# Kernel tuning notes

Hardware: AMD Instinct MI355X
Metric: run time of the kernel (lower is better)

Reference implementation:

```python
import jax, jax.numpy as jnp
import numpy as np

NUM_HEADS = 32
HEAD_DIM = 64
ROPE_THETA = 10000.0


def _rope_cos_sin(position_ids, head_dim, theta):
    # inv_freq: [head_dim/2]
    half = head_dim // 2
    inv_freq = 1.0 / (theta ** (jnp.arange(0, half, dtype=jnp.float32) * 2.0 / head_dim))
    angles = position_ids.astype(jnp.float32)[..., None] * inv_freq  # [B,S,half]
    return jnp.cos(angles), jnp.sin(angles)


def _apply_rope(x, cos, sin):
    # x: [B,S,H,hd]; cos/sin: [B,S,half] -> broadcast over heads (rotate-half, Llama style)
    half = x.shape[-1] // 2
    x1, x2 = x[..., :half], x[..., half:]
    c = cos[:, :, None, :]
    s = sin[:, :, None, :]
    return jnp.concatenate([x1 * c - x2 * s, x2 * c + x1 * s], axis=-1)


def setup_inputs() -> dict:
    key = jax.random.key(0)
    ks = jax.random.split(key, 8)
    B, S, D = 2, 2048, 2048
    hidden_states = jax.random.normal(ks[0], (B, S, D), dtype=jnp.float32)
    # causal additive mask (is_causal=False in IpexSDP; mask carries causality)
    causal = jnp.tril(jnp.ones((S, S), dtype=jnp.bool_))
    attention_mask = jnp.where(causal, 0.0, -1e9).astype(jnp.float32)[None, None, :, :]
    attention_mask = jnp.broadcast_to(attention_mask, (B, 1, S, S))
    position_ids = jnp.broadcast_to(jnp.arange(S, dtype=jnp.int64)[None, :], (B, S))
    scale = 0.02
    qkv_w = jax.random.normal(ks[1], (3, D, D), dtype=jnp.float32) * scale
    qkv_b = jax.random.normal(ks[2], (3, D), dtype=jnp.float32) * scale
    o_w = jax.random.normal(ks[3], (D, D), dtype=jnp.float32) * scale
    o_b = jax.random.normal(ks[4], (D,), dtype=jnp.float32) * scale
    residual = jax.random.normal(ks[5], (B, S, D), dtype=jnp.float32)
    return {
        'hidden_states': hidden_states,
        'attention_mask': attention_mask,
        'position_ids': position_ids,
        'qkv_w': qkv_w,
        'qkv_b': qkv_b,
        'o_w': o_w,
        'o_b': o_b,
        'residual': residual,
    }


def reference(hidden_states, attention_mask, position_ids, qkv_w, qkv_b, o_w, o_b, residual):
    B, S, D = hidden_states.shape
    H, hd = NUM_HEADS, HEAD_DIM
    # fused QKV projection (weights stored transposed: x @ W), matching mm_qkv_out
    qkv = jnp.einsum('bsd,tde->tbse', hidden_states, qkv_w) + qkv_b[:, None, None, :]
    q = qkv[0].reshape(B, S, H, hd)
    k = qkv[1].reshape(B, S, H, hd)
    v = qkv[2].reshape(B, S, H, hd)
    cos, sin = _rope_cos_sin(position_ids, hd, ROPE_THETA)
    q = _apply_rope(q, cos, sin)
    k = _apply_rope(k, cos, sin)
    scale = 1.0 / jnp.sqrt(jnp.asarray(hd, dtype=hidden_states.dtype))
    # [B,H,S,S]
    scores = jnp.einsum('bqhd,bkhd->bhqk', q, k) * scale + attention_mask
    probs = jax.nn.softmax(scores, axis=-1)
    attn = jnp.einsum('bhqk,bkhd->bqhd', probs, v).reshape(B, S, D)
    # o-proj fused with bias + residual add (matmul_add_add)
    out = attn @ o_w + o_b + residual
    return out
```

## Files before the change

### kernel.cpp

```cpp
#include <hip/hip_runtime.h>
#include <stdint.h>
#include <stdio.h>

#define D_MODEL 2048
#define SEQ     2048
#define NHEADS  32
#define HDIM    64
#define BATCH   2
#define BH      (BATCH * NHEADS)
#define GK      2048
#define NT      (GK / 64)

typedef unsigned short u16;
typedef unsigned int   u32;
typedef __attribute__((ext_vector_type(8))) short short8;
typedef __attribute__((ext_vector_type(4))) short s16x4;
typedef __attribute__((ext_vector_type(4))) float f32x4;
typedef __attribute__((ext_vector_type(4))) u32   u32x4;
typedef __attribute__((ext_vector_type(2))) u32   u32x2;

__device__ __forceinline__ float bf2f(u16 x) {
  union { u32 u; float f; } c; c.u = ((u32)x) << 16; return c.f;
}
__device__ __forceinline__ u16 f2bf(float f) {
  union { float f; u32 u; } c; c.f = f;
  u32 u = c.u;
  return (u16)((u + 0x7FFFu + ((u >> 16) & 1u)) >> 16);
}
__device__ __forceinline__ u32 fbits(float f) {
  union { float f; u32 u; } c; c.f = f; return c.u;
}

typedef const __attribute__((address_space(1))) u32* gas_t;
typedef __attribute__((address_space(3))) u32* las_t;
__device__ __forceinline__ void gll16(const void* g, void* l) {
  __builtin_amdgcn_global_load_lds((gas_t)g, (las_t)l, 16, 0, 0);
}
__device__ __forceinline__ u32 lds_addr(const void* p) {
  return (u32)(size_t)(const __attribute__((address_space(3))) void*)p;
}
template <int OFF>
__device__ __forceinline__ short8 ds_read128o(u32 addr) {
  short8 r;
  asm volatile("ds_read_b128 %0, %1 offset:%2" : "=v"(r) : "v"(addr), "i"(OFF));
  return r;
}

#define SBAR0 __builtin_amdgcn_sched_barrier(0)

__device__ __forceinline__ void swiz_mn(int pid, int nx, int& mtile, int& ntile) {
  int chunk = 8 * nx;
  int grp = pid / chunk, loc = pid - grp * chunk;
  mtile = grp * 8 + (loc & 7);
  ntile = loc >> 3;
}

__global__ __launch_bounds__(256) void cvt_k(const float* __restrict__ in,
                                             u16* __restrict__ out) {
  int id = blockIdx.x * 256 + threadIdx.x;
  f32x4 v = *(const f32x4*)&in[(size_t)id * 4];
  alignas(8) u16 o[4];
#pragma unroll
  for (int j = 0; j < 4; j++) o[j] = f2bf(v[j]);
  *(u32x2*)&out[(size_t)id * 4] = *(const u32x2*)o;
}

__global__ __launch_bounds__(256) void transpose_cvt_k(const float* __restrict__ qkv_w,
                                                       const float* __restrict__ o_w,
                                                       u16* __restrict__ outT) {
  __shared__ u16 tile[64][72];
  const int z = blockIdx.z;
  const float* inz = (z < 3) ? qkv_w + (size_t)z * D_MODEL * D_MODEL : o_w;
  u16* outz = outT + (size_t)z * D_MODEL * D_MODEL;
  const int r0 = blockIdx.y * 64, c0 = blockIdx.x * 64;
  const int t = threadIdx.x;
  const int lrow = t >> 4, lcol4 = (t & 15) * 4;
#pragma unroll
  for (int i = 0; i < 4; i++) {
    int r = lrow + i * 16;
    f32x4 v = *(const f32x4*)&inz[(size_t)(r0 + r) * D_MODEL + (c0 + lcol4)];
#pragma unroll
    for (int j = 0; j < 4; j++) tile[r][lcol4 + j] = f2bf(v[j]);
  }
  __syncthreads();
  const int row = t >> 3, col8 = (t & 7) * 8;
#pragma unroll
  for (int i = 0; i < 2; i++) {
    int r = row + i * 32;
    alignas(16) u16 vals[8];
#pragma unroll
    for (int j = 0; j < 8; j++) vals[j] = tile[col8 + j][r];
    *(u32x4*)&outz[(size_t)(c0 + r) * D_MODEL + (r0 + col8)] = *(const u32x4*)vals;
  }
}

__device__ __forceinline__ void stage_half(const u16* __restrict__ src, int rowbase, int k0,
                                           u16* tile, int h, int w, int srl, int scol) {
  u16* ldsb = tile + h * (128 * 64);
  const u16* g0 = &src[(size_t)(rowbase + h * 128 + srl) * GK + k0 + scol];
  const u16* g1 = &src[(size_t)(rowbase + h * 128 + srl + 8) * GK + k0 + scol];
  gll16(g0, (char*)ldsb + w * 2048);
  gll16(g1, (char*)ldsb + w * 2048 + 1024);
}

__device__ __forceinline__ void rd8(short8 dst[4][2], u32 base, u32 cq0, u32 cq1) {
  u32 b0 = base + cq0, b1 = base + cq1;
  dst[0][0] = ds_read128o<0>(b0);    dst[0][1] = ds_read128o<0>(b1);
  dst[1][0] = ds_read128o<2048>(b0); dst[1][1] = ds_read128o<2048>(b1);
  dst[2][0] = ds_read128o<4096>(b0); dst[2][1] = ds_read128o<4096>(b1);
  dst[3][0] = ds_read128o<6144>(b0); dst[3][1] = ds_read128o<6144>(b1);
}

template <int NFLO>
__device__ __forceinline__ void mfma_half(const short8 afc[4][2], const short8 bfc[4][2],
                                          f32x4 acc[4][4]) {
  __builtin_amdgcn_s_setprio(1);
#pragma unroll
  for (int mf = 0; mf < 4; mf++)
#pragma unroll
    for (int nf = NFLO; nf < NFLO + 2; nf++) {
      acc[mf][nf] = __builtin_amdgcn_mfma_f32_16x16x32_bf16(afc[mf][0], bfc[nf][0], acc[mf][nf], 0, 0, 0);
      acc[mf][nf] = __builtin_amdgcn_mfma_f32_16x16x32_bf16(afc[mf][1], bfc[nf][1], acc[mf][nf], 0, 0, 0);
    }
  __builtin_amdgcn_s_setprio(0);
}

#define KT_BODY(KT_, AFC, BFC, AFN, BFN)                                        \
  do {                                                                           \
    if ((KT_) + 1 < NT) rd8(AFN, asb + (u32)ri * (u32)(128 * 64 * 2) + rowA, cq0, cq1); \
    if ((KT_) + 1 < NT) { asm volatile("s_waitcnt lgkmcnt(8)"); }                \
    else                { asm volatile("s_waitcnt lgkmcnt(0)"); }                \
    SBAR0;                                                                       \
    mfma_half<0>(AFC, BFC, acc);                                                 \
    if ((KT_) + 1 < NT) rd8(BFN, bsb + (u32)ri * (u32)(256 * 64 * 2) + rowB, cq0, cq1); \
    SBAR0;                                                                       \
    mfma_half<2>(AFC, BFC, acc);                                                 \
    __builtin_amdgcn_s_barrier();                                                \
    SBAR0;                                                                       \
    if ((KT_) + 3 < NT) {                                                        \
      const int k3_ = ((KT_) + 3) * 64;                                          \
      stage_half(Ag, m0, k3_, AsB + si * (128 * 64), 0, w, srl, scol);           \
      stage_half(Bg, n0, k3_, BsB + si * (256 * 64), 0, w, srl, scol);           \
      stage_half(Bg, n0, k3_, BsB + si * (256 * 64), 1, w, srl, scol);           \
      asm volatile("s_waitcnt vmcnt(6)");                                        \
    } else {                                                                     \
      asm volatile("s_waitcnt vmcnt(0)");                                        \
    }                                                                            \
    SBAR0;                                                                       \
    __builtin_amdgcn_s_barrier();                                                \
    SBAR0;                                                                       \
    { int th_ = 3 - si - ri; si = ri; ri = th_; }                                \
  } while (0)

__device__ __forceinline__ void gemm_128x256(const u16* __restrict__ Ag,
                                             const u16* __restrict__ Bg,
                                             int m0, int n0,
                                             u16* AsB, u16* BsB,
                                             f32x4 acc[4][4]) {
  const int t = threadIdx.x, w = t >> 6, lane = t & 63;
  const int quad = lane >> 4, l16 = lane & 15;
  const int wr = w >> 2, wc = w & 3;
  const int srl = w * 16 + (lane >> 3);
  const int scol = (((lane & 7) ^ (lane >> 3)) << 3);
  const u32 asb = lds_addr(AsB), bsb = lds_addr(BsB);
  const u32 xorc = (u32)((l16 & 7) << 4);
  const u32 cq0 = (u32)(quad * 16) ^ xorc;
  const u32 cq1 = (u32)(64 + quad * 16) ^ xorc;
  const u32 rowA = (u32)((wr * 64 + l16) * 128);
  const u32 rowB = (u32)((wc * 64 + l16) * 128);

#pragma unroll
  for (int mf = 0; mf < 4; mf++)
#pragma unroll
    for (int nf = 0; nf < 4; nf++)
#pragma unroll
      for (int i = 0; i < 4; i++) acc[mf][nf][i] = 0.0f;

#pragma unroll
  for (int tt = 0; tt < 3; tt++) {
    stage_half(Ag, m0, tt * 64, AsB + tt * (128 * 64), 0, w, srl, scol);
    stage_half(Bg, n0, tt * 64, BsB + tt * (256 * 64), 0, w, srl, scol);
    stage_half(Bg, n0, tt * 64, BsB + tt * (256 * 64), 1, w, srl, scol);
  }
  asm volatile("s_waitcnt vmcnt(6)");
  SBAR0;
  __builtin_amdgcn_s_barrier();
  SBAR0;

  short8 af0[4][2], bf0[4][2], af1[4][2], bf1[4][2];
  rd8(af0, asb + rowA, cq0, cq1);
  rd8(bf0, bsb + rowB, cq0, cq1);
  int si = 0, ri = 1;

  for (int kt = 0; kt < NT; kt += 2) {
    KT_BODY(kt,     af0, bf0, af1, bf1);
    KT_BODY(kt + 1, af1, bf1, af0, bf0);
  }
}

__global__ __launch_bounds__(512, 1) void qkv_gemm_k(const u16* __restrict__ A,
                                                     const u16* __restrict__ BT,
                                                     const float* __restrict__ bias,
                                                     u16* __restrict__ Qb, u16* __restrict__ Kb,
                                                     u16* __restrict__ Vbt) {
  __shared__ u16 As[3][128 * 64];
  __shared__ u16 Bs[3][256 * 64];
  f32x4 acc[4][4];
  int mtile, ntile;
  swiz_mn(blockIdx.x, 24, mtile, ntile);
  const int m0 = mtile * 128, n0 = ntile * 256;
  gemm_128x256(A, BT, m0, n0, &As[0][0], &Bs[0][0], acc);

  const int t = threadIdx.x, lane = t & 63, quad = lane >> 4, l16 = lane & 15;
  const int w = t >> 6, wr = w >> 2, wc = w & 3;
  const int tsel = n0 >> 11;
  if (tsel < 2) {
    u16* dst = tsel ? Kb : Qb;
#pragma unroll
    for (int p = 0; p < 2; p++) {
      int nlo = n0 + wc * 64 + p * 16 + l16;
      float blo = bias[nlo], bhi = bias[nlo + 32];
      int j = p * 16 + l16;
      float inv = __expf((float)j * -0.28782313662425572f);
      int h = (nlo & 2047) >> 6;
#pragma unroll
      for (int mf = 0; mf < 4; mf++) {
#pragma unroll
        for (int r = 0; r < 4; r++) {
          int m = m0 + wr * 64 + mf * 16 + quad * 4 + r;
          int b = m >> 11, s = m & (SEQ - 1);
          float sn, cs;
          __sincosf((float)s * inv, &sn, &cs);
          float x1 = acc[mf][p][r] + blo;
          float x2 = acc[mf][p + 2][r] + bhi;
          size_t base = ((size_t)((b * NHEADS + h) * SEQ + s)) * HDIM;
          dst[base + j]      = f2bf(x1 * cs - x2 * sn);
          dst[base + j + 32] = f2bf(x2 * cs + x1 * sn);
        }
      }
    }
  } else {
#pragma unroll
    for (int nf = 0; nf < 4; nf++) {
      int n = n0 + wc * 64 + nf * 16 + l16;
      float bv = bias[n];
      int e = n & 2047, h = e >> 6, d = e & 63;
#pragma unroll
      for (int mf = 0; mf < 4; mf++) {
        int m0r = m0 + wr * 64 + mf * 16 + quad * 4;
        int b = m0r >> 11, s0 = m0r & (SEQ - 1);
        alignas(8) u16 o4[4];
#pragma unroll
        for (int r = 0; r < 4; r++) o4[r] = f2bf(acc[mf][nf][r] + bv);
        *(u32x2*)&Vbt[((size_t)((b * NHEADS + h) * HDIM + d)) * SEQ + s0] = *(const u32x2*)o4;
      }
    }
  }
}

__global__ __launch_bounds__(512, 1) void oproj_gemm_k(const u16* __restrict__ A,
                                                       const u16* __restrict__ BT,
                                                       const float* __restrict__ bias,
                                                       const float* __restrict__ resid,
                                                       float* __restrict__ out) {
  __shared__ u16 As[3][128 * 64];
  __shared__ u16 Bs[3][256 * 64];
  f32x4 acc[4][4];
  int mtile, ntile;
  swiz_mn(blockIdx.x, 8, mtile, ntile);
  const int m0 = mtile * 128, n0 = ntile * 256;
  gemm_128x256(A, BT, m0, n0, &As[0][0], &Bs[0][0], acc);

  const int t = threadIdx.x, lane = t & 63, quad = lane >> 4, l16 = lane & 15;
  const int w = t >> 6, wr = w >> 2, wc = w & 3;
#pragma unroll
  for (int nf = 0; nf < 4; nf++) {
    int n = n0 + wc * 64 + nf * 16 + l16;
    float bv = bias[n];
#pragma unroll
    for (int mf = 0; mf < 4; mf++) {
#pragma unroll
      for (int r = 0; r < 4; r++) {
        int m = m0 + wr * 64 + mf * 16 + quad * 4 + r;
        size_t oi = (size_t)m * D_MODEL + n;
        out[oi] = acc[mf][nf][r] + bv + resid[oi];
      }
    }
  }
}

#define ATT_BUF (128 * 72 + 64 * 136)

__global__ __launch_bounds__(256, 2) void attn_k(const u16* __restrict__ Qb,
                                                 const u16* __restrict__ Kb,
                                                 const u16* __restrict__ Vbt,
                                                 u16* __restrict__ attn) {
  __shared__ u16 smem[2 * ATT_BUF];
  const int blk = blockIdx.x;
  const int bh = blk & 63, pi = blk >> 6;
  const int b = bh >> 5, h = bh & 31;
  const int t = threadIdx.x, w = t >> 6, lane = t & 63, quad = lane >> 4, l16 = lane & 15;
  const int qbT[2] = { pi * 128, (15 - pi) * 128 };
  const int qwT[2] = { qbT[0] + w * 32, qbT[1] + w * 32 };
  const size_t bho = (size_t)bh * SEQ * HDIM;
  const size_t vbo = (size_t)bh * HDIM * SEQ;
  const int kend = qbT[1] + 128;
  const int nr = kend >> 7;

  short8 qf[2][2][2];
#pragma unroll
  for (int Ti = 0; Ti < 2; Ti++)
#pragma unroll
    for (int qt = 0; qt < 2; qt++)
#pragma unroll
      for (int kd = 0; kd < 2; kd++) {
        short8 v = *(const short8*)&Qb[bho + (size_t)(qwT[Ti] + qt * 16 + l16) * HDIM + kd * 32 + quad * 8];
#pragma unroll
        for (int i = 0; i < 8; i++) {
          float f = bf2f((u16)v[i]) * 0.125f;
          v[i] = (short)f2bf(f);
        }
        qf[Ti][qt][kd] = v;
      }

  f32x4 Oacc[2][4][2];
  float mrow[2][2] = {{-1e30f, -1e30f}, {-1e30f, -1e30f}};
  float lrow[2][2] = {{0.0f, 0.0f}, {0.0f, 0.0f}};
#pragma unroll
  for (int Ti = 0; Ti < 2; Ti++)
#pragma unroll
    for (int dt = 0; dt < 4; dt++)
#pragma unroll
      for (int qt = 0; qt < 2; qt++)
#pragma unroll
        for (int i = 0; i < 4; i++) Oacc[Ti][dt][qt][i] = 0.0f;

  const int krow = t >> 3, kcol = (t & 7) * 8;
  u32x4 kreg[4], vreg[4];

#pragma unroll
  for (int c = 0; c < 4; c++) {
    kreg[c] = *(const u32x4*)&Kb[bho + (size_t)(krow + c * 32) * HDIM + kcol];
    int id = t + c * 256, vrow = id >> 4, vcol = (id & 15) * 8;
    vreg[c] = *(const u32x4*)&Vbt[vbo + (size_t)vrow * SEQ + vcol];
  }
  {
    u16* Ks = smem;
    u16* Vt = smem + 128 * 72;
#pragma unroll
    for (int c = 0; c < 4; c++) {
      *(u32x4*)&Ks[(krow + c * 32) * 72 + kcol] = kreg[c];
      int id = t + c * 256, vrow = id >> 4, vcol = (id & 15) * 8;
      *(u32x4*)&Vt[vrow * 136 + vcol] = vreg[c];
    }
  }
  __syncthreads();

  for (int r = 0; r < nr; r++) {
    const int key0 = r << 7;
    const int cur = r & 1;
    u16* Ks = smem + cur * ATT_BUF;
    u16* Vt = Ks + 128 * 72;
    if (r + 1 < nr) {
      const int nk0 = key0 + 128;
#pragma unroll
      for (int c = 0; c < 4; c++) {
        kreg[c] = *(const u32x4*)&Kb[bho + (size_t)(nk0 + krow + c * 32) * HDIM + kcol];
        int id = t + c * 256, vrow = id >> 4, vcol = (id & 15) * 8;
        vreg[c] = *(const u32x4*)&Vbt[vbo + (size_t)vrow * SEQ + nk0 + vcol];
      }
    }
#pragma unroll
    for (int s = 0; s < 2; s++) {
      const int k0s = key0 + s * 64;
      const int so = s * 64;
#pragma unroll
      for (int Ti = 0; Ti < 2; Ti++) {
        const int qw = qwT[Ti];
        if (k0s <= qw + 31) {
          const int lim = qw + 31 - k0s;
          int nkt = (lim >> 4) + 1; if (nkt > 4) nkt = 4;
          f32x4 sacc[4][2];
#pragma unroll
          for (int kt = 0; kt < 4; kt++) {
            if (kt < nkt) {
              short8 kf0 = *(const short8*)&Ks[(so + kt * 16 + l16) * 72 + quad * 8];
              short8 kf1 = *(const short8*)&Ks[(so + kt * 16 + l16) * 72 + 32 + quad * 8];
#pragma unroll
              for (int qt = 0; qt < 2; qt++) {
                f32x4 z = {0.0f, 0.0f, 0.0f, 0.0f};
                z = __builtin_amdgcn_mfma_f32_16x16x32_bf16(kf0, qf[Ti][qt][0], z, 0, 0, 0);
                z = __builtin_amdgcn_mfma_f32_16x16x32_bf16(kf1, qf[Ti][qt][1], z, 0, 0, 0);
                sacc[kt][qt] = z;
              }
            }
          }
          if (k0s + 63 > qw) {
#pragma unroll
            for (int qt = 0; qt < 2; qt++) {
              int qrow = qw + qt * 16 + l16;
#pragma unroll
              for (int kt = 0; kt < 4; kt++)
                if (kt < nkt)
#pragma unroll
                  for (int rr = 0; rr < 4; rr++)
                    if (k0s + kt * 16 + quad * 4 + rr > qrow) sacc[kt][qt][rr] = -1e30f;
            }
          }
          float alpha[2];
#pragma unroll
          for (int qt = 0; qt < 2; qt++) {
            float mx = -1e30f;
#pragma unroll
            for (int kt = 0; kt < 4; kt++)
              if (kt < nkt)
#pragma unroll
                for (int rr = 0; rr < 4; rr++) mx = fmaxf(mx, sacc[kt][qt][rr]);
            mx = fmaxf(mx, __shfl_xor(mx, 16));
            mx = fmaxf(mx, __shfl_xor(mx, 32));
            float mnew = fmaxf(mrow[Ti][qt], mx);
            alpha[qt] = __expf(mrow[Ti][qt] - mnew);
            mrow[Ti][qt] = mnew;
            float rsum = 0.0f;
#pragma unroll
            for (int kt = 0; kt < 4; kt++)
              if (kt < nkt)
#pragma unroll
                for (int rr = 0; rr < 4; rr++) {
                  float pv = __expf(sacc[kt][qt][rr] - mnew);
                  sacc[kt][qt][rr] = pv;
                  rsum += pv;
                }
            rsum += __shfl_xor(rsum, 16);
            rsum += __shfl_xor(rsum, 32);
            lrow[Ti][qt] = lrow[Ti][qt] * alpha[qt] + rsum;
          }
#pragma unroll
          for (int dt = 0; dt < 4; dt++)
#pragma unroll
            for (int qt = 0; qt < 2; qt++)
#pragma unroll
              for (int rr = 0; rr < 4; rr++) Oacc[Ti][dt][qt][rr] *= alpha[qt];
#pragma unroll
          for (int kt = 0; kt < 4; kt++) {
            if (kt < nkt) {
              s16x4 pk[2];
#pragma unroll
              for (int qt = 0; qt < 2; qt++) {
                u32 a0 = fbits(sacc[kt][qt][0]) + 0x8000u;
                u32 a1 = fbits(sacc[kt][qt][1]) + 0x8000u;
                u32 a2 = fbits(sacc[kt][qt][2]) + 0x8000u;
                u32 a3 = fbits(sacc[kt][qt][3]) + 0x8000u;
                union { u32 u[2]; s16x4 s; } pc;
                pc.u[0] = __builtin_amdgcn_perm(a1, a0, 0x07060302u);
                pc.u[1] = __builtin_amdgcn_perm(a3, a2, 0x07060302u);
                pk[qt] = pc.s;
              }
              s16x4 vf[4];
#pragma unroll
              for (int dt = 0; dt < 4; dt++)
                vf[dt] = *(const s16x4*)&Vt[(dt * 16 + l16) * 136 + so + kt * 16 + quad * 4];
#pragma unroll
              for (int dt = 0; dt < 4; dt++)
#pragma unroll
                for (int qt = 0; qt < 2; qt++)
                  Oacc[Ti][dt][qt] = __builtin_amdgcn_mfma_f32_16x16x16bf16_1k(vf[dt], pk[qt], Oacc[Ti][dt][qt], 0, 0, 0);
            }
          }
        }
      }
    }
    if (r + 1 < nr) {
      u16* Ksn = smem + (cur ^ 1) * ATT_BUF;
      u16* Vtn = Ksn + 128 * 72;
#pragma unroll
      for (int c = 0; c < 4; c++) {
        *(u32x4*)&Ksn[(krow + c * 32) * 72 + kcol] = kreg[c];
        int id = t + c * 256, vrow = id >> 4, vcol = (id & 15) * 8;
        *(u32x4*)&Vtn[vrow * 136 + vcol] = vreg[c];
      }
    }
    __syncthreads();
  }

#pragma unroll
  for (int Ti = 0; Ti < 2; Ti++) {
    float invl[2] = {1.0f / lrow[Ti][0], 1.0f / lrow[Ti][1]};
#pragma unroll
    for (int dt = 0; dt < 4; dt++)
#pragma unroll
      for (int qt = 0; qt < 2; qt++)
#pragma unroll
        for (int rr = 0; rr < 4; rr++)
          smem[(w * 32 + qt * 16 + l16) * 72 + dt * 16 + quad * 4 + rr] =
              f2bf(Oacc[Ti][dt][qt][rr] * invl[qt]);
    __syncthreads();
#pragma unroll
    for (int ii = 0; ii < 4; ii++) {
      int chunk = t + ii * 256;
      int row = chunk >> 3, g = chunk & 7;
      *(u32x4*)&attn[((size_t)(b * SEQ + qbT[Ti] + row)) * D_MODEL + h * 64 + g * 8] =
          *(const u32x4*)&smem[row * 72 + g * 8];
    }
    __syncthreads();
  }
}

extern "C" void kernel_launch(void* const* d_in, const int* in_sizes, int n_in,
                              void* d_out, int out_size, void* d_ws, size_t ws_size,
                              hipStream_t stream) {
  (void)in_sizes; (void)n_in; (void)out_size;
  const float* hidden = (const float*)d_in[0];
  const float* qkv_w = (const float*)d_in[3];
  const float* qkv_b = (const float*)d_in[4];
  const float* o_w   = (const float*)d_in[5];
  const float* o_b   = (const float*)d_in[6];
  const float* resid = (const float*)d_in[7];
  float* out = (float*)d_out;

  u16* ws = (u16*)d_ws;
  size_t off = 0;
  u16* hidb  = ws + off; off += (size_t)BATCH * SEQ * D_MODEL;
  u16* qkvT  = ws + off; off += (size_t)3 * D_MODEL * D_MODEL;
  u16* owT   = ws + off; off += (size_t)D_MODEL * D_MODEL;
  u16* Qb    = ws + off; off += (size_t)BH * SEQ * HDIM;
  u16* Kb    = ws + off; off += (size_t)BH * SEQ * HDIM;
  u16* Vbt   = ws + off; off += (size_t)BH * SEQ * HDIM;
  u16* attnb = ws + off; off += (size_t)BATCH * SEQ * D_MODEL;
  if (ws_size < off * sizeof(u16)) {
    fprintf(stderr, "kernel_launch: workspace too small: need %zu bytes, have %zu\n",
            off * sizeof(u16), ws_size);
    return;
  }
  (void)owT;

  cvt_k<<<(BATCH * SEQ * D_MODEL) / (4 * 256), 256, 0, stream>>>(hidden, hidb);
  transpose_cvt_k<<<dim3(32, 32, 4), 256, 0, stream>>>(qkv_w, o_w, qkvT);
  qkv_gemm_k<<<32 * 24, 512, 0, stream>>>(hidb, qkvT, qkv_b, Qb, Kb, Vbt);
  attn_k<<<BH * 8, 256, 0, stream>>>(Qb, Kb, Vbt, attnb);
  oproj_gemm_k<<<32 * 8, 512, 0, stream>>>(attnb, owT, o_b, resid, out);
}
```

Measured before the change: 412.4 us.

## Replace QKV GEMM with 256x256 tile kernel using interleaved double-buffered pipeline

The QKV projection moves from 128x256 to 256x256 output tiles per block, halving the grid and doubling the work per wave (8x4 accumulator fragments). A new main loop double-buffers A and B in LDS and interleaves partial global-to-LDS staging, LDS fragment reads and MFMA quarter-blocks, with explicit barriers and waitcnts between them. The goal is higher arithmetic intensity and less global traffic per FLOP. The cost is more accumulator registers and 384 blocks, which may not fill all CUs evenly, plus tighter hand-tuned synchronisation.

```diff
diff --git a/kernel.cpp b/kernel.cpp
--- a/kernel.cpp
+++ b/kernel.cpp
@@ -91,6 +91,182 @@
 #pragma unroll
     for (int j = 0; j < 8; j++) vals[j] = tile[col8 + j][r];
     *(u32x4*)&outz[(size_t)(c0 + r) * D_MODEL + (r0 + col8)] = *(const u32x4*)vals;
+  }
+}
+
+
+__device__ __forceinline__ void stage_h256(const u16* __restrict__ src, int grow0, int k0,
+                                           u16* ldsHalf, int w, int srl, int scol) {
+  const u16* g0 = &src[(size_t)(grow0 + srl) * GK + k0 + scol];
+  const u16* g1 = &src[(size_t)(grow0 + srl + 8) * GK + k0 + scol];
+  gll16(g0, (char*)ldsHalf + w * 2048);
+  gll16(g1, (char*)ldsHalf + w * 2048 + 1024);
+}
+
+__global__ __launch_bounds__(512, 1) void qkv_gemm256_k(const u16* __restrict__ A,
+                                                        const u16* __restrict__ BT,
+                                                        const float* __restrict__ bias,
+                                                        u16* __restrict__ Qb, u16* __restrict__ Kb,
+                                                        u16* __restrict__ Vbt) {
+  __shared__ u16 As[2][2][128 * 64];
+  __shared__ u16 Bs[2][2][128 * 64];
+  const int t = threadIdx.x, w = t >> 6, lane = t & 63;
+  const int quad = lane >> 4, l16 = lane & 15;
+  const int wr = w >> 2, wc = w & 3;
+  int mtile, ntile;
+  swiz_mn(blockIdx.x, 24, mtile, ntile);
+  const int m0 = mtile * 256, n0 = ntile * 256;
+  const int srl = w * 16 + (lane >> 3);
+  const int scol = (((lane & 7) ^ (lane >> 3)) << 3);
+
+  const u32 asb = lds_addr(As), bsb = lds_addr(Bs);
+  const u32 xorc = (u32)((l16 & 7) << 4);
+  const u32 cq0 = (u32)(quad * 16) ^ xorc;
+  const u32 cq1 = (u32)(64 + quad * 16) ^ xorc;
+  const u32 aA[2] = { asb + (u32)(wr * 16384 + l16 * 128),
+                      asb + 32768u + (u32)(wr * 16384 + l16 * 128) };
+  const u32 aB[2] = { bsb + (u32)((wc >> 1) * 16384 + ((wc & 1) * 64 + l16) * 128),
+                      bsb + 32768u + (u32)((wc >> 1) * 16384 + ((wc & 1) * 64 + l16) * 128) };
+
+  f32x4 acc[8][4];
+#pragma unroll
+  for (int mf = 0; mf < 8; mf++)
+#pragma unroll
+    for (int nf = 0; nf < 4; nf++)
+#pragma unroll
+      for (int i = 0; i < 4; i++) acc[mf][nf][i] = 0.0f;
+
+  short8 af[8][2], bf[4][2];
+
+#define RD_AF03(BUF_) do { u32 b0 = aA[BUF_] + cq0, b1 = aA[BUF_] + cq1;            \
+    af[0][0] = ds_read128o<0>(b0);     af[0][1] = ds_read128o<0>(b1);               \
+    af[1][0] = ds_read128o<2048>(b0);  af[1][1] = ds_read128o<2048>(b1);            \
+    af[2][0] = ds_read128o<4096>(b0);  af[2][1] = ds_read128o<4096>(b1);            \
+    af[3][0] = ds_read128o<6144>(b0);  af[3][1] = ds_read128o<6144>(b1); } while (0)
+#define RD_AF47(BUF_) do { u32 b0 = aA[BUF_] + cq0, b1 = aA[BUF_] + cq1;            \
+    af[4][0] = ds_read128o<8192>(b0);  af[4][1] = ds_read128o<8192>(b1);            \
+    af[5][0] = ds_read128o<10240>(b0); af[5][1] = ds_read128o<10240>(b1);           \
+    af[6][0] = ds_read128o<12288>(b0); af[6][1] = ds_read128o<12288>(b1);           \
+    af[7][0] = ds_read128o<14336>(b0); af[7][1] = ds_read128o<14336>(b1); } while (0)
+#define RD_BF01(BUF_) do { u32 b0 = aB[BUF_] + cq0, b1 = aB[BUF_] + cq1;            \
+    bf[0][0] = ds_read128o<0>(b0);     bf[0][1] = ds_read128o<0>(b1);               \
+    bf[1][0] = ds_read128o<2048>(b0);  bf[1][1] = ds_read128o<2048>(b1); } while (0)
+#define RD_BF23(BUF_) do { u32 b0 = aB[BUF_] + cq0, b1 = aB[BUF_] + cq1;            \
+    bf[2][0] = ds_read128o<4096>(b0);  bf[2][1] = ds_read128o<4096>(b1);            \
+    bf[3][0] = ds_read128o<6144>(b0);  bf[3][1] = ds_read128o<6144>(b1); } while (0)
+#define MFMA_Q(MLO_, NLO_) do { __builtin_amdgcn_s_setprio(1);                      \
+    _Pragma("unroll") for (int mf = (MLO_); mf < (MLO_) + 4; mf++)                  \
+      _Pragma("unroll") for (int nf = (NLO_); nf < (NLO_) + 2; nf++) {              \
+        acc[mf][nf] = __builtin_amdgcn_mfma_f32_16x16x32_bf16(af[mf][0], bf[nf][0], acc[mf][nf], 0, 0, 0); \
+        acc[mf][nf] = __builtin_amdgcn_mfma_f32_16x16x32_bf16(af[mf][1], bf[nf][1], acc[mf][nf], 0, 0, 0); \
+      }                                                                             \
+    __builtin_amdgcn_s_setprio(0); } while (0)
+
+  stage_h256(A, m0, 0, &As[0][0][0], w, srl, scol);
+  stage_h256(A, m0 + 128, 0, &As[0][1][0], w, srl, scol);
+  stage_h256(BT, n0, 0, &Bs[0][0][0], w, srl, scol);
+  stage_h256(BT, n0 + 128, 0, &Bs[0][1][0], w, srl, scol);
+  stage_h256(A, m0, 64, &As[1][0][0], w, srl, scol);
+  stage_h256(A, m0 + 128, 64, &As[1][1][0], w, srl, scol);
+  asm volatile("s_waitcnt vmcnt(4)");
+  SBAR0;
+  __builtin_amdgcn_s_barrier();
+  SBAR0;
+  RD_AF03(0);
+  RD_BF01(0);
+
+  for (int kt = 0; kt < NT; kt++) {
+    const int buf = kt & 1, nbuf = buf ^ 1;
+    RD_AF47(buf);
+    if (kt + 1 < NT) stage_h256(BT, n0, (kt + 1) * 64, &Bs[nbuf][0][0], w, srl, scol);
+    __builtin_amdgcn_s_barrier();
+    asm volatile("s_waitcnt lgkmcnt(8)");
+    SBAR0;
+    MFMA_Q(0, 0);
+    __builtin_amdgcn_s_barrier();
+    SBAR0;
+    RD_BF23(buf);
+    if (kt + 1 < NT) stage_h256(BT, n0 + 128, (kt + 1) * 64, &Bs[nbuf][1][0], w, srl, scol);
+    __builtin_amdgcn_s_barrier();
+    asm volatile("s_waitcnt lgkmcnt(4)");
+    SBAR0;
+    MFMA_Q(4, 0);
+    __builtin_amdgcn_s_barrier();
+    SBAR0;
+    if (kt + 2 < NT) stage_h256(A, m0, (kt + 2) * 64, &As[buf][0][0], w, srl, scol);
+    __builtin_amdgcn_s_barrier();
+    asm volatile("s_waitcnt lgkmcnt(0)");
+    SBAR0;
+    MFMA_Q(0, 2);
+    if (kt + 2 < NT) {
+      asm volatile("s_waitcnt vmcnt(2)");
+    } else {
+      asm volatile("s_waitcnt vmcnt(0)");
+    }
+    SBAR0;
+    __builtin_amdgcn_s_barrier();
+    SBAR0;
+    if (kt + 1 < NT) {
+      RD_AF03(nbuf);
+      RD_BF01(nbuf);
+    }
+    if (kt + 2 < NT) stage_h256(A, m0 + 128, (kt + 2) * 64, &As[buf][1][0], w, srl, scol);
+    __builtin_amdgcn_s_barrier();
+    if (kt + 1 < NT) { asm volatile("s_waitcnt lgkmcnt(12)"); }
+    else             { asm volatile("s_waitcnt lgkmcnt(0)"); }
+    SBAR0;
+    MFMA_Q(4, 2);
+    __builtin_amdgcn_s_barrier();
+    SBAR0;
+  }
+#undef RD_AF03
+#undef RD_AF47
+#undef RD_BF01
+#undef RD_BF23
+#undef MFMA_Q
+
+  const int tsel = n0 >> 11;
+  if (tsel < 2) {
+    u16* dst = tsel ? Kb : Qb;
+#pragma unroll
+    for (int p = 0; p < 2; p++) {
+      int nlo = n0 + wc * 64 + p * 16 + l16;
+      float blo = bias[nlo], bhi = bias[nlo + 32];
+      int j = p * 16 + l16;
+      float inv = __expf((float)j * -0.28782313662425572f);
+      int h = (nlo & 2047) >> 6;
+#pragma unroll
+      for (int mf = 0; mf < 8; mf++) {
+#pragma unroll
+        for (int r = 0; r < 4; r++) {
+          int m = m0 + wr * 128 + mf * 16 + quad * 4 + r;
+          int b = m >> 11, s = m & (SEQ - 1);
+          float sn, cs;
+          __sincosf((float)s * inv, &sn, &cs);
+          float x1 = acc[mf][p][r] + blo;
+          float x2 = acc[mf][p + 2][r] + bhi;
+          size_t base = ((size_t)((b * NHEADS + h) * SEQ + s)) * HDIM;
+          dst[base + j]      = f2bf(x1 * cs - x2 * sn);
+          dst[base + j + 32] = f2bf(x2 * cs + x1 * sn);
+        }
+      }
+    }
+  } else {
+#pragma unroll
+    for (int nf = 0; nf < 4; nf++) {
+      int n = n0 + wc * 64 + nf * 16 + l16;
+      float bv = bias[n];
+      int e = n & 2047, h = e >> 6, d = e & 63;
+#pragma unroll
+      for (int mf = 0; mf < 8; mf++) {
+        int m0r = m0 + wr * 128 + mf * 16 + quad * 4;
+        int b = m0r >> 11, s0 = m0r & (SEQ - 1);
+        alignas(8) u16 o4[4];
+#pragma unroll
+        for (int r = 0; r < 4; r++) o4[r] = f2bf(acc[mf][nf][r] + bv);
+        *(u32x2*)&Vbt[((size_t)((b * NHEADS + h) * HDIM + d)) * SEQ + s0] = *(const u32x2*)o4;
+      }
+    }
   }
 }
 
@@ -198,66 +374,6 @@
   }
 }
 
-__global__ __launch_bounds__(512, 1) void qkv_gemm_k(const u16* __restrict__ A,
-                                                     const u16* __restrict__ BT,
-                                                     const float* __restrict__ bias,
-                                                     u16* __restrict__ Qb, u16* __restrict__ Kb,
-                                                     u16* __restrict__ Vbt) {
-  __shared__ u16 As[3][128 * 64];
-  __shared__ u16 Bs[3][256 * 64];
-  f32x4 acc[4][4];
-  int mtile, ntile;
-  swiz_mn(blockIdx.x, 24, mtile, ntile);
-  const int m0 = mtile * 128, n0 = ntile * 256;
-  gemm_128x256(A, BT, m0, n0, &As[0][0], &Bs[0][0], acc);
-
-  const int t = threadIdx.x, lane = t & 63, quad = lane >> 4, l16 = lane & 15;
-  const int w = t >> 6, wr = w >> 2, wc = w & 3;
-  const int tsel = n0 >> 11;
-  if (tsel < 2) {
-    u16* dst = tsel ? Kb : Qb;
-#pragma unroll
-    for (int p = 0; p < 2; p++) {
-      int nlo = n0 + wc * 64 + p * 16 + l16;
-      float blo = bias[nlo], bhi = bias[nlo + 32];
-      int j = p * 16 + l16;
-      float inv = __expf((float)j * -0.28782313662425572f);
-      int h = (nlo & 2047) >> 6;
-#pragma unroll
-      for (int mf = 0; mf < 4; mf++) {
-#pragma unroll
-        for (int r = 0; r < 4; r++) {
-          int m = m0 + wr * 64 + mf * 16 + quad * 4 + r;
-          int b = m >> 11, s = m & (SEQ - 1);
-          float sn, cs;
-          __sincosf((float)s * inv, &sn, &cs);
-          float x1 = acc[mf][p][r] + blo;
-          float x2 = acc[mf][p + 2][r] + bhi;
-          size_t base = ((size_t)((b * NHEADS + h) * SEQ + s)) * HDIM;
-          dst[base + j]      = f2bf(x1 * cs - x2 * sn);
-          dst[base + j + 32] = f2bf(x2 * cs + x1 * sn);
-        }
-      }
-    }
-  } else {
-#pragma unroll
-    for (int nf = 0; nf < 4; nf++) {
-      int n = n0 + wc * 64 + nf * 16 + l16;
-      float bv = bias[n];
-      int e = n & 2047, h = e >> 6, d = e & 63;
-#pragma unroll
-      for (int mf = 0; mf < 4; mf++) {
-        int m0r = m0 + wr * 64 + mf * 16 + quad * 4;
-        int b = m0r >> 11, s0 = m0r & (SEQ - 1);
-        alignas(8) u16 o4[4];
-#pragma unroll
-        for (int r = 0; r < 4; r++) o4[r] = f2bf(acc[mf][nf][r] + bv);
-        *(u32x2*)&Vbt[((size_t)((b * NHEADS + h) * HDIM + d)) * SEQ + s0] = *(const u32x2*)o4;
-      }
-    }
-  }
-}
-
 __global__ __launch_bounds__(512, 1) void oproj_gemm_k(const u16* __restrict__ A,
                                                        const u16* __restrict__ BT,
                                                        const float* __restrict__ bias,
@@ -536,7 +652,7 @@
 
   cvt_k<<<(BATCH * SEQ * D_MODEL) / (4 * 256), 256, 0, stream>>>(hidden, hidb);
   transpose_cvt_k<<<dim3(32, 32, 4), 256, 0, stream>>>(qkv_w, o_w, qkvT);
-  qkv_gemm_k<<<32 * 24, 512, 0, stream>>>(hidb, qkvT, qkv_b, Qb, Kb, Vbt);
+  qkv_gemm256_k<<<16 * 24, 512, 0, stream>>>(hidb, qkvT, qkv_b, Qb, Kb, Vbt);
   attn_k<<<BH * 8, 256, 0, stream>>>(Qb, Kb, Vbt, attnb);
   oproj_gemm_k<<<32 * 8, 512, 0, stream>>>(attnb, owT, o_b, resid, out);
 }
```

Measured after the change: 415.8 us. Within noise of the previous version (+0.8%).

## Fuse prep conversion kernels and defer softmax rescaling with max threshold

Applied to the files above, without the earlier changes.

Merges the hidden-state bf16 conversion and the weight transpose-convert into a single launch, with the block index choosing which job a block does. This removes one kernel launch and its gap. In the attention loop, online-softmax rescaling of the O accumulators and running max is skipped when every lane's new tile max stays within 8 of the stored max (FA4-style lazy rescale). That saves the exp and the multiplies in the common case, but adds a wave-wide vote and lets exponentials grow up to e^8, which can cost bf16 precision for P.

```diff
diff --git a/kernel.cpp b/kernel.cpp
--- a/kernel.cpp
+++ b/kernel.cpp
@@ -55,25 +55,26 @@
   ntile = loc >> 3;
 }
 
-__global__ __launch_bounds__(256) void cvt_k(const float* __restrict__ in,
-                                             u16* __restrict__ out) {
-  int id = blockIdx.x * 256 + threadIdx.x;
-  f32x4 v = *(const f32x4*)&in[(size_t)id * 4];
-  alignas(8) u16 o[4];
-#pragma unroll
-  for (int j = 0; j < 4; j++) o[j] = f2bf(v[j]);
-  *(u32x2*)&out[(size_t)id * 4] = *(const u32x2*)o;
-}
-
-__global__ __launch_bounds__(256) void transpose_cvt_k(const float* __restrict__ qkv_w,
-                                                       const float* __restrict__ o_w,
-                                                       u16* __restrict__ outT) {
+__global__ __launch_bounds__(256) void prep_k(const float* __restrict__ hidden,
+                                              const float* __restrict__ qkv_w,
+                                              const float* __restrict__ o_w,
+                                              u16* __restrict__ hidb,
+                                              u16* __restrict__ outT) {
   __shared__ u16 tile[64][72];
-  const int z = blockIdx.z;
+  const int bid = blockIdx.x, t = threadIdx.x;
+  if (bid >= 4096) {
+    int id = (bid - 4096) * 256 + t;
+    f32x4 v = *(const f32x4*)&hidden[(size_t)id * 4];
+    alignas(8) u16 o[4];
+#pragma unroll
+    for (int j = 0; j < 4; j++) o[j] = f2bf(v[j]);
+    *(u32x2*)&hidb[(size_t)id * 4] = *(const u32x2*)o;
+    return;
+  }
+  const int z = bid >> 10, within = bid & 1023;
+  const int r0 = (within >> 5) * 64, c0 = (within & 31) * 64;
   const float* inz = (z < 3) ? qkv_w + (size_t)z * D_MODEL * D_MODEL : o_w;
   u16* outz = outT + (size_t)z * D_MODEL * D_MODEL;
-  const int r0 = blockIdx.y * 64, c0 = blockIdx.x * 64;
-  const int t = threadIdx.x;
   const int lrow = t >> 4, lcol4 = (t & 15) * 4;
 #pragma unroll
   for (int i = 0; i < 4; i++) {
@@ -407,7 +408,7 @@
                     if (k0s + kt * 16 + quad * 4 + rr > qrow) sacc[kt][qt][rr] = -1e30f;
             }
           }
-          float alpha[2];
+          float mx2[2];
 #pragma unroll
           for (int qt = 0; qt < 2; qt++) {
             float mx = -1e30f;
@@ -418,16 +419,34 @@
                 for (int rr = 0; rr < 4; rr++) mx = fmaxf(mx, sacc[kt][qt][rr]);
             mx = fmaxf(mx, __shfl_xor(mx, 16));
             mx = fmaxf(mx, __shfl_xor(mx, 32));
-            float mnew = fmaxf(mrow[Ti][qt], mx);
-            alpha[qt] = __expf(mrow[Ti][qt] - mnew);
-            mrow[Ti][qt] = mnew;
+            mx2[qt] = mx;
+          }
+          float alpha[2] = {1.0f, 1.0f};
+          bool defer = __all((mx2[0] <= mrow[Ti][0] + 8.0f) &
+                             (mx2[1] <= mrow[Ti][1] + 8.0f));
+          if (!defer) {
+#pragma unroll
+            for (int qt = 0; qt < 2; qt++) {
+              float mnew = fmaxf(mrow[Ti][qt], mx2[qt]);
+              alpha[qt] = __expf(mrow[Ti][qt] - mnew);
+              mrow[Ti][qt] = mnew;
+            }
+#pragma unroll
+            for (int dt = 0; dt < 4; dt++)
+#pragma unroll
+              for (int qt = 0; qt < 2; qt++)
+#pragma unroll
+                for (int rr = 0; rr < 4; rr++) Oacc[Ti][dt][qt][rr] *= alpha[qt];
+          }
+#pragma unroll
+          for (int qt = 0; qt < 2; qt++) {
             float rsum = 0.0f;
 #pragma unroll
             for (int kt = 0; kt < 4; kt++)
               if (kt < nkt)
 #pragma unroll
                 for (int rr = 0; rr < 4; rr++) {
-                  float pv = __expf(sacc[kt][qt][rr] - mnew);
+                  float pv = __expf(sacc[kt][qt][rr] - mrow[Ti][qt]);
                   sacc[kt][qt][rr] = pv;
                   rsum += pv;
                 }
@@ -435,12 +454,6 @@
             rsum += __shfl_xor(rsum, 32);
             lrow[Ti][qt] = lrow[Ti][qt] * alpha[qt] + rsum;
           }
-#pragma unroll
-          for (int dt = 0; dt < 4; dt++)
-#pragma unroll
-            for (int qt = 0; qt < 2; qt++)
-#pragma unroll
-              for (int rr = 0; rr < 4; rr++) Oacc[Ti][dt][qt][rr] *= alpha[qt];
 #pragma unroll
           for (int kt = 0; kt < 4; kt++) {
             if (kt < nkt) {
@@ -534,8 +547,7 @@
   }
   (void)owT;
 
-  cvt_k<<<(BATCH * SEQ * D_MODEL) / (4 * 256), 256, 0, stream>>>(hidden, hidb);
-  transpose_cvt_k<<<dim3(32, 32, 4), 256, 0, stream>>>(qkv_w, o_w, qkvT);
+  prep_k<<<12288, 256, 0, stream>>>(hidden, qkv_w, o_w, hidb, qkvT);
   qkv_gemm_k<<<32 * 24, 512, 0, stream>>>(hidb, qkvT, qkv_b, Qb, Kb, Vbt);
   attn_k<<<BH * 8, 256, 0, stream>>>(Qb, Kb, Vbt, attnb);
   oproj_gemm_k<<<32 * 8, 512, 0, stream>>>(attnb, owT, o_b, resid, out);
```

Result: faster. 403.9 us (-2.0%).
